# Optimization experiments

Hardware: AMD Instinct MI355X
Metric: run time of the kernel (lower is better)

The kernel has to match this reference:

```python
import jax, jax.numpy as jnp
import numpy as np

N = 50000      # nodes
E = 800000     # edges (before self-loops)
IN = 64        # in_channels
HID = 128      # hidden_channels
EPS = 1e-5     # BatchNorm eps


def _bn(x, g, b):
    # eval-mode BatchNorm with running_mean=0, running_var=1
    return x * (g / np.float32(np.sqrt(1.0 + EPS))) + b


def _gat(x, src, dst, W, a_s, a_d, bias, heads, outc):
    # PyG GATConv: lin -> per-node attention logits -> edge softmax over dst -> scatter-sum
    n = x.shape[0]
    xh = (x @ W).reshape(n, heads, outc)                    # [N,H,C]
    al_s = (xh * a_s[None]).sum(-1)                          # [N,H]
    al_d = (xh * a_d[None]).sum(-1)                          # [N,H]
    alpha = jax.nn.leaky_relu(al_s[src] + al_d[dst], 0.2)    # [E2,H]
    amax = jax.ops.segment_max(alpha, dst, num_segments=n)   # segment softmax (stable)
    ex = jnp.exp(alpha - amax[dst])
    den = jax.ops.segment_sum(ex, dst, num_segments=n)
    w = ex / den[dst]                                        # [E2,H]
    out = jax.ops.segment_sum(xh[src] * w[:, :, None], dst, num_segments=n)
    return out.reshape(n, heads * outc) + bias


def setup_inputs() -> dict:
    key = jax.random.key(0)
    ks = jax.random.split(key, 40)
    nrm = lambda k, s, sc=0.05: jax.random.normal(k, s, jnp.float32) * sc
    inp = {}
    inp['x'] = jax.random.normal(ks[0], (N, IN), jnp.float32)
    inp['edge_index'] = jax.random.randint(ks[1], (2, E), 0, N, dtype=jnp.int64)
    inp['Wp'] = nrm(ks[2], (IN, HID)); inp['bp'] = jnp.zeros((HID,), jnp.float32)
    # layer 0/1: heads=4, out=32; layer 2: heads=1, out=128
    C4 = HID // 4
    inp['W0'] = nrm(ks[3], (HID, HID)); inp['as0'] = nrm(ks[4], (4, C4)); inp['ad0'] = nrm(ks[5], (4, C4)); inp['b0'] = jnp.zeros((HID,), jnp.float32)
    inp['g0'] = jnp.ones((HID,), jnp.float32); inp['be0'] = jnp.zeros((HID,), jnp.float32)
    inp['W1'] = nrm(ks[6], (HID, HID)); inp['as1'] = nrm(ks[7], (4, C4)); inp['ad1'] = nrm(ks[8], (4, C4)); inp['b1'] = jnp.zeros((HID,), jnp.float32)
    inp['g1'] = jnp.ones((HID,), jnp.float32); inp['be1'] = jnp.zeros((HID,), jnp.float32)
    inp['W2'] = nrm(ks[9], (HID, HID)); inp['as2'] = nrm(ks[10], (1, HID)); inp['ad2'] = nrm(ks[11], (1, HID)); inp['b2'] = jnp.zeros((HID,), jnp.float32)
    inp['g2'] = jnp.ones((HID,), jnp.float32); inp['be2'] = jnp.zeros((HID,), jnp.float32)
    inp['fi'] = jnp.ones((HID,), jnp.float32)
    inp['Wc1'] = nrm(ks[12], (HID, HID // 2)); inp['bc1'] = jnp.zeros((HID // 2,), jnp.float32)
    inp['gc'] = jnp.ones((HID // 2,), jnp.float32); inp['bec'] = jnp.zeros((HID // 2,), jnp.float32)
    inp['Wc2'] = nrm(ks[13], (HID // 2, HID // 4)); inp['bc2'] = jnp.zeros((HID // 4,), jnp.float32)
    inp['Wc3'] = nrm(ks[14], (HID // 4, 2)); inp['bc3'] = jnp.zeros((2,), jnp.float32)
    return inp


def reference(x, edge_index, Wp, bp, W0, as0, ad0, b0, g0, be0, W1, as1, ad1, b1, g1, be1, W2, as2, ad2, b2, g2, be2, fi, Wc1, bc1, gc, bec, Wc2, bc2, Wc3, bc3):
    n = x.shape[0]
    loops = jnp.arange(n, dtype=edge_index.dtype)  # GATConv add_self_loops=True
    src = jnp.concatenate([edge_index[0], loops])
    dst = jnp.concatenate([edge_index[1], loops])
    h = x @ Wp + bp
    h = jax.nn.elu(_bn(_gat(h, src, dst, W0, as0, ad0, b0, 4, HID // 4), g0, be0))
    h = jax.nn.elu(_bn(_gat(h, src, dst, W1, as1, ad1, b1, 4, HID // 4), g1, be1))
    h = jax.nn.elu(_bn(_gat(h, src, dst, W2, as2, ad2, b2, 1, HID), g2, be2))
    h = h * fi
    h = jax.nn.relu(h @ Wc1 + bc1)
    h = _bn(h, gc, bec)
    h = jax.nn.relu(h @ Wc2 + bc2)
    return h @ Wc3 + bc3
```

## Files before the change

kernel.cpp:

```cpp
#include <hip/hip_runtime.h>
#include <math.h>

#define NFEAT 128
#define INF   64
#define BN_RSQ 0.99999500003749937f

template <int K, int NT, int EPI>
__launch_bounds__(256)
__global__ void linear4_kernel(const float* __restrict__ in, const float* __restrict__ W,
                               const float* __restrict__ bias, const float* __restrict__ g,
                               const float* __restrict__ be, float* __restrict__ out, int n) {
    __shared__ float xs[64 * 68];
    __shared__ float wsm[64 * 68];
    const int tx = threadIdx.x & 15;
    const int ty = threadIdx.x >> 4;
    const int row0 = blockIdx.x * 64;
    const int col0 = blockIdx.y * 64;
    float acc[4][4] = {};
    for (int kc = 0; kc < K; kc += 64) {
        __syncthreads();
        for (int i = threadIdx.x; i < 1024; i += 256) {
            const int rr = i >> 4;
            const int k4 = (i & 15) << 2;
            const int row = row0 + rr;
            float4 v = make_float4(0.f, 0.f, 0.f, 0.f);
            if (row < n) v = *(const float4*)&in[(long)row * K + kc + k4];
            *(float4*)&xs[rr * 68 + k4] = v;
        }
        for (int i = threadIdx.x; i < 1024; i += 256) {
            const int kk = i >> 4;
            const int j4 = (i & 15) << 2;
            *(float4*)&wsm[kk * 68 + j4] =
                *(const float4*)&W[(long)(kc + kk) * NT + col0 + j4];
        }
        __syncthreads();
#pragma unroll 16
        for (int k = 0; k < 64; ++k) {
            const float4 wv = *(const float4*)&wsm[k * 68 + (tx << 2)];
            const float x0 = xs[(ty * 4 + 0) * 68 + k];
            const float x1 = xs[(ty * 4 + 1) * 68 + k];
            const float x2 = xs[(ty * 4 + 2) * 68 + k];
            const float x3 = xs[(ty * 4 + 3) * 68 + k];
            acc[0][0] = fmaf(x0, wv.x, acc[0][0]); acc[0][1] = fmaf(x0, wv.y, acc[0][1]);
            acc[0][2] = fmaf(x0, wv.z, acc[0][2]); acc[0][3] = fmaf(x0, wv.w, acc[0][3]);
            acc[1][0] = fmaf(x1, wv.x, acc[1][0]); acc[1][1] = fmaf(x1, wv.y, acc[1][1]);
            acc[1][2] = fmaf(x1, wv.z, acc[1][2]); acc[1][3] = fmaf(x1, wv.w, acc[1][3]);
            acc[2][0] = fmaf(x2, wv.x, acc[2][0]); acc[2][1] = fmaf(x2, wv.y, acc[2][1]);
            acc[2][2] = fmaf(x2, wv.z, acc[2][2]); acc[2][3] = fmaf(x2, wv.w, acc[2][3]);
            acc[3][0] = fmaf(x3, wv.x, acc[3][0]); acc[3][1] = fmaf(x3, wv.y, acc[3][1]);
            acc[3][2] = fmaf(x3, wv.z, acc[3][2]); acc[3][3] = fmaf(x3, wv.w, acc[3][3]);
        }
    }
    const int col = col0 + (tx << 2);
    float4 bv = make_float4(0.f, 0.f, 0.f, 0.f);
    if (bias) bv = *(const float4*)&bias[col];
    float4 gv, ev;
    if (EPI == 2) { gv = *(const float4*)&g[col]; ev = *(const float4*)&be[col]; }
#pragma unroll
    for (int i = 0; i < 4; ++i) {
        const int row = row0 + ty * 4 + i;
        if (row >= n) break;
        float4 v = make_float4(acc[i][0] + bv.x, acc[i][1] + bv.y,
                               acc[i][2] + bv.z, acc[i][3] + bv.w);
        if (EPI == 2) {
            v.x = fmaxf(v.x, 0.f) * (gv.x * BN_RSQ) + ev.x;
            v.y = fmaxf(v.y, 0.f) * (gv.y * BN_RSQ) + ev.y;
            v.z = fmaxf(v.z, 0.f) * (gv.z * BN_RSQ) + ev.z;
            v.w = fmaxf(v.w, 0.f) * (gv.w * BN_RSQ) + ev.w;
        }
        *(float4*)&out[(long)row * NT + col] = v;
    }
}

template <int K, int MT, int MFULL, int EPI, int ITERS>
__launch_bounds__(256)
__global__ void linear_kernel(const float* __restrict__ in, const float* __restrict__ W,
                              const float* __restrict__ bias, float* __restrict__ out, int n) {
    constexpr int RPI = 256 / MT;
    __shared__ float Wl[K * MT];
    __shared__ float xl[RPI * (K + 1)];
    for (int i = threadIdx.x; i < K * MT; i += 256)
        Wl[i] = W[(i / MT) * MFULL + (i % MT)];
    const int j = threadIdx.x % MT;
    const int r = threadIdx.x / MT;
    const int row0 = blockIdx.x * (RPI * ITERS);
    for (int it = 0; it < ITERS; ++it) {
        const int base = row0 + it * RPI;
        __syncthreads();
        for (int i = threadIdx.x; i < RPI * K; i += 256) {
            int rr = i / K, kk = i - rr * K;
            int row = base + rr;
            xl[rr * (K + 1) + kk] = (row < n) ? in[(long)row * K + kk] : 0.f;
        }
        __syncthreads();
        float acc = 0.f;
#pragma unroll
        for (int k = 0; k < K; ++k) acc += xl[r * (K + 1) + k] * Wl[k * MT + j];
        const int row = base + r;
        if (row < n) {
            float v = acc;
            if (bias) v += bias[j];
            if (EPI >= 1) v = fmaxf(v, 0.f);
            out[(long)row * MFULL + j] = v;
        }
    }
}

template <int H, int C>
__global__ void gat_logits_kernel(const float* __restrict__ xh, const float* __restrict__ a_s,
                                  const float* __restrict__ a_d, float* __restrict__ als,
                                  float* __restrict__ ald, int n) {
    int idx = blockIdx.x * blockDim.x + threadIdx.x;
    if (idx >= n * H) return;
    int node = idx / H, h = idx - node * H;
    const float4* xp  = (const float4*)(xh + (long)node * NFEAT + h * C);
    const float4* asp = (const float4*)(a_s + h * C);
    const float4* adp = (const float4*)(a_d + h * C);
    float ss = 0.f, sd = 0.f;
#pragma unroll
    for (int c = 0; c < C / 4; ++c) {
        float4 v = xp[c], a = asp[c], b = adp[c];
        ss += v.x * a.x + v.y * a.y + v.z * a.z + v.w * a.w;
        sd += v.x * b.x + v.y * b.y + v.z * b.z + v.w * b.w;
    }
    als[idx] = ss;
    ald[idx] = sd;
}

__global__ void zero_int_kernel(int* __restrict__ p, int n) {
    int i = blockIdx.x * blockDim.x + threadIdx.x;
    if (i < n) p[i] = 0;
}

__global__ void hist_kernel(const int* __restrict__ ei, int E, int n, int* __restrict__ deg) {
    int e = blockIdx.x * blockDim.x + threadIdx.x;
    if (e >= E + n) return;
    int d = (e < E) ? ei[E + e] : (e - E);
    atomicAdd(&deg[d], 1);
}

__global__ void scanA_kernel(const int* __restrict__ deg, int n,
                             int* __restrict__ rowptr, int* __restrict__ bsum) {
    __shared__ int s[256];
    int t = threadIdx.x;
    int idx = blockIdx.x * 256 + t;
    s[t] = (idx < n) ? deg[idx] : 0;
    __syncthreads();
    for (int o = 1; o < 256; o <<= 1) {
        int x = (t >= o) ? s[t - o] : 0;
        __syncthreads();
        s[t] += x;
        __syncthreads();
    }
    if (idx < n) rowptr[idx + 1] = s[t];
    if (t == 255) bsum[blockIdx.x] = s[255];
}

__global__ void scanB_kernel(int* __restrict__ bsum, int nb) {
    __shared__ int s[256];
    int t = threadIdx.x;
    s[t] = (t < nb) ? bsum[t] : 0;
    __syncthreads();
    for (int o = 1; o < 256; o <<= 1) {
        int x = (t >= o) ? s[t - o] : 0;
        __syncthreads();
        s[t] += x;
        __syncthreads();
    }
    if (t < nb) bsum[t] = s[t];
}

__global__ void scanC_kernel(const int* __restrict__ deg, int n, int* __restrict__ rowptr,
                             const int* __restrict__ bsum, int* __restrict__ cursor) {
    int idx = blockIdx.x * 256 + threadIdx.x;
    if (idx >= n) return;
    int off = (blockIdx.x > 0) ? bsum[blockIdx.x - 1] : 0;
    int val = rowptr[idx + 1] + off;
    rowptr[idx + 1] = val;
    cursor[idx] = val - deg[idx];
    if (idx == 0) rowptr[0] = 0;
}

__global__ void scatter_kernel(const int* __restrict__ ei, int E, int n,
                               int* __restrict__ cursor, int* __restrict__ csr_src) {
    int e = blockIdx.x * blockDim.x + threadIdx.x;
    if (e >= E + n) return;
    int s, d;
    if (e < E) { s = ei[e]; d = ei[E + e]; } else { s = e - E; d = s; }
    int pos = atomicAdd(&cursor[d], 1);
    csr_src[pos] = s;
}

template <int H>
__launch_bounds__(256)
__global__ void gat_gather_kernel(const int* __restrict__ rowptr, const int* __restrict__ csr_src,
                                  const float* __restrict__ xh, const float* __restrict__ als,
                                  const float* __restrict__ ald, const float* __restrict__ bias,
                                  const float* __restrict__ g, const float* __restrict__ be,
                                  const float* __restrict__ post, float* __restrict__ hout, int n) {
    const int lane = threadIdx.x & 63;
    const int d = blockIdx.x * 4 + (threadIdx.x >> 6);
    if (d >= n) return;
    const int c0 = lane, c1 = lane + 64;
    const int h0 = (H == 4) ? (lane >> 5) : 0;
    const int h1 = (H == 4) ? (h0 + 2) : 0;
    const float ad0 = ald[d * H + h0];
    const float ad1 = ald[d * H + h1];
    const int rs = rowptr[d], re = rowptr[d + 1];
    float den0 = 0.f, den1 = 0.f, acc0 = 0.f, acc1 = 0.f;
    for (int base = rs; base < re; base += 64) {
        int sv = 0;
        if (base + lane < re) sv = csr_src[base + lane];
        const int cnt = min(64, re - base);
        int s = __shfl(sv, 0, 64);
        float a0 = als[s * H + h0];
        float a1 = als[s * H + h1];
        float x0 = xh[(long)s * NFEAT + c0];
        float x1 = xh[(long)s * NFEAT + c1];
        for (int t = 0; t < cnt; ++t) {
            const float ca0 = a0, ca1 = a1, cx0 = x0, cx1 = x1;
            if (t + 1 < cnt) {
                const int sn = __shfl(sv, t + 1, 64);
                a0 = als[sn * H + h0];
                a1 = als[sn * H + h1];
                x0 = xh[(long)sn * NFEAT + c0];
                x1 = xh[(long)sn * NFEAT + c1];
            }
            float l0 = ca0 + ad0, l1 = ca1 + ad1;
            l0 = l0 > 0.f ? l0 : 0.2f * l0;
            l1 = l1 > 0.f ? l1 : 0.2f * l1;
            const float w0 = __expf(l0), w1 = __expf(l1);
            den0 += w0;                den1 += w1;
            acc0 = fmaf(w0, cx0, acc0); acc1 = fmaf(w1, cx1, acc1);
        }
    }
    float v0 = (acc0 / den0 + bias[c0]) * (g[c0] * BN_RSQ) + be[c0];
    float v1 = (acc1 / den1 + bias[c1]) * (g[c1] * BN_RSQ) + be[c1];
    v0 = v0 > 0.f ? v0 : expm1f(v0);
    v1 = v1 > 0.f ? v1 : expm1f(v1);
    if (post) { v0 *= post[c0]; v1 *= post[c1]; }
    hout[(long)d * NFEAT + c0] = v0;
    hout[(long)d * NFEAT + c1] = v1;
}

template <int H>
static void run_gat_layer(const float* hin, float* xh, float* als, float* ald,
                          const int* rowptr, const int* csr_src, int n,
                          const float* W, const float* as_, const float* ad_, const float* b,
                          const float* g, const float* be, const float* post, float* hout,
                          hipStream_t stream) {
    constexpr int C = NFEAT / H;
    dim3 grid((n + 63) / 64, 2);
    linear4_kernel<128, 128, 0><<<grid, 256, 0, stream>>>(hin, W, nullptr, nullptr, nullptr, xh, n);
    gat_logits_kernel<H, C><<<(n * H + 255) / 256, 256, 0, stream>>>(xh, as_, ad_, als, ald, n);
    gat_gather_kernel<H><<<(n + 3) / 4, 256, 0, stream>>>(rowptr, csr_src, xh, als, ald,
                                                          b, g, be, post, hout, n);
}

extern "C" void kernel_launch(void* const* d_in, const int* in_sizes, int n_in,
                              void* d_out, int out_size, void* d_ws, size_t ws_size,
                              hipStream_t stream) {
    const float* x   = (const float*)d_in[0];
    const int*   ei  = (const int*)d_in[1];
    const float* Wp  = (const float*)d_in[2];
    const float* bp  = (const float*)d_in[3];
    const float* W0  = (const float*)d_in[4];
    const float* as0 = (const float*)d_in[5];
    const float* ad0 = (const float*)d_in[6];
    const float* b0  = (const float*)d_in[7];
    const float* g0  = (const float*)d_in[8];
    const float* be0 = (const float*)d_in[9];
    const float* W1  = (const float*)d_in[10];
    const float* as1 = (const float*)d_in[11];
    const float* ad1 = (const float*)d_in[12];
    const float* b1  = (const float*)d_in[13];
    const float* g1  = (const float*)d_in[14];
    const float* be1 = (const float*)d_in[15];
    const float* W2  = (const float*)d_in[16];
    const float* as2 = (const float*)d_in[17];
    const float* ad2 = (const float*)d_in[18];
    const float* b2  = (const float*)d_in[19];
    const float* g2  = (const float*)d_in[20];
    const float* be2 = (const float*)d_in[21];
    const float* fi  = (const float*)d_in[22];
    const float* Wc1 = (const float*)d_in[23];
    const float* bc1 = (const float*)d_in[24];
    const float* gc  = (const float*)d_in[25];
    const float* bec = (const float*)d_in[26];
    const float* Wc2 = (const float*)d_in[27];
    const float* bc2 = (const float*)d_in[28];
    const float* Wc3 = (const float*)d_in[29];
    const float* bc3 = (const float*)d_in[30];

    const int n  = in_sizes[0] / INF;
    const int E  = in_sizes[1] / 2;
    const int E2 = E + n;
    const int NB = (n + 255) / 256;

    float* ws   = (float*)d_ws;
    float* h    = ws;
    float* xh   = h + (long)n * NFEAT;
    float* als  = xh + (long)n * NFEAT;
    float* ald  = als + (long)n * 4;
    int* deg     = (int*)(ald + (long)n * 4);
    int* rowptr  = deg + n;
    int* cursor  = rowptr + (n + 1);
    int* csr_src = cursor + n;
    int* bsum    = csr_src + (long)E2;

    zero_int_kernel<<<NB, 256, 0, stream>>>(deg, n);
    hist_kernel<<<(E2 + 255) / 256, 256, 0, stream>>>(ei, E, n, deg);
    scanA_kernel<<<NB, 256, 0, stream>>>(deg, n, rowptr, bsum);
    scanB_kernel<<<1, 256, 0, stream>>>(bsum, NB);
    scanC_kernel<<<NB, 256, 0, stream>>>(deg, n, rowptr, bsum, cursor);
    scatter_kernel<<<(E2 + 255) / 256, 256, 0, stream>>>(ei, E, n, cursor, csr_src);

    {
        dim3 grid((n + 63) / 64, 2);
        linear4_kernel<64, 128, 0><<<grid, 256, 0, stream>>>(x, Wp, bp, nullptr, nullptr, h, n);
    }

    run_gat_layer<4>(h, xh, als, ald, rowptr, csr_src, n, W0, as0, ad0, b0, g0, be0, nullptr, h, stream);
    run_gat_layer<4>(h, xh, als, ald, rowptr, csr_src, n, W1, as1, ad1, b1, g1, be1, nullptr, h, stream);
    run_gat_layer<1>(h, xh, als, ald, rowptr, csr_src, n, W2, as2, ad2, b2, g2, be2, fi, h, stream);

    {
        dim3 grid((n + 63) / 64, 1);
        linear4_kernel<128, 64, 2><<<grid, 256, 0, stream>>>(h, Wc1, bc1, gc, bec, xh, n);
    }
    linear_kernel<64, 32, 32, 1, 8><<<(n + 63) / 64, 256, 0, stream>>>(xh, Wc2, bc2, h, n);
    linear_kernel<32, 2, 2, 0, 2><<<(n + 255) / 256, 256, 0, stream>>>(h, Wc3, bc3, (float*)d_out, n);
}
```

Measured before the change: 645.2 us.

## Precompute edge weights per lane in LDS and add 128x128 register-tiled GEMM

After: 633.1 us. Within noise of the previous version (-1.9%).

```diff
diff --git a/kernel.cpp b/kernel.cpp
--- a/kernel.cpp
+++ b/kernel.cpp
@@ -4,6 +4,73 @@
 #define NFEAT 128
 #define INF   64
 #define BN_RSQ 0.99999500003749937f
+
+template <int K>
+__launch_bounds__(256)
+__global__ void linear8_kernel(const float* __restrict__ in, const float* __restrict__ W,
+                               const float* __restrict__ bias, float* __restrict__ out, int n) {
+    __shared__ float xs[128 * 36];
+    __shared__ float wt[128 * 36];
+    const int tid = threadIdx.x;
+    const int tx = tid & 15;
+    const int ty = tid >> 4;
+    const int row0 = blockIdx.x * 128;
+    float acc[8][8] = {};
+    for (int kc = 0; kc < K; kc += 32) {
+        __syncthreads();
+#pragma unroll
+        for (int r = 0; r < 4; ++r) {
+            const int idx = tid + 256 * r;
+            const int rr = idx >> 3;
+            const int k4 = (idx & 7) << 2;
+            const int row = row0 + rr;
+            float4 v = make_float4(0.f, 0.f, 0.f, 0.f);
+            if (row < n) v = *(const float4*)&in[(long)row * K + kc + k4];
+            *(float4*)&xs[rr * 36 + k4] = v;
+        }
+#pragma unroll
+        for (int r = 0; r < 4; ++r) {
+            const int idx = tid + 256 * r;
+            const int kk = idx >> 5;
+            const int c4 = (idx & 31) << 2;
+            const float4 v = *(const float4*)&W[(long)(kc + kk) * 128 + c4];
+            wt[(c4 + 0) * 36 + kk] = v.x;
+            wt[(c4 + 1) * 36 + kk] = v.y;
+            wt[(c4 + 2) * 36 + kk] = v.z;
+            wt[(c4 + 3) * 36 + kk] = v.w;
+        }
+        __syncthreads();
+#pragma unroll 2
+        for (int k4 = 0; k4 < 32; k4 += 4) {
+            float4 xa[8], wa[8];
+#pragma unroll
+            for (int i = 0; i < 8; ++i) xa[i] = *(const float4*)&xs[(ty + 16 * i) * 36 + k4];
+#pragma unroll
+            for (int j = 0; j < 8; ++j) wa[j] = *(const float4*)&wt[(tx + 16 * j) * 36 + k4];
+#pragma unroll
+            for (int i = 0; i < 8; ++i)
+#pragma unroll
+                for (int j = 0; j < 8; ++j) {
+                    acc[i][j] = fmaf(xa[i].x, wa[j].x, acc[i][j]);
+                    acc[i][j] = fmaf(xa[i].y, wa[j].y, acc[i][j]);
+                    acc[i][j] = fmaf(xa[i].z, wa[j].z, acc[i][j]);
+                    acc[i][j] = fmaf(xa[i].w, wa[j].w, acc[i][j]);
+                }
+        }
+    }
+#pragma unroll
+    for (int i = 0; i < 8; ++i) {
+        const int row = row0 + ty + 16 * i;
+        if (row >= n) continue;
+#pragma unroll
+        for (int j = 0; j < 8; ++j) {
+            const int col = tx + 16 * j;
+            float v = acc[i][j];
+            if (bias) v += bias[col];
+            out[(long)row * 128 + col] = v;
+        }
+    }
+}
 
 template <int K, int NT, int EPI>
 __launch_bounds__(256)
@@ -198,40 +265,65 @@
                                   const float* __restrict__ ald, const float* __restrict__ bias,
                                   const float* __restrict__ g, const float* __restrict__ be,
                                   const float* __restrict__ post, float* __restrict__ hout, int n) {
+    __shared__ int   slds[4][64];
+    __shared__ float wlds[4][64][H];
     const int lane = threadIdx.x & 63;
-    const int d = blockIdx.x * 4 + (threadIdx.x >> 6);
+    const int wid  = threadIdx.x >> 6;
+    const int d = blockIdx.x * 4 + wid;
     if (d >= n) return;
     const int c0 = lane, c1 = lane + 64;
     const int h0 = (H == 4) ? (lane >> 5) : 0;
     const int h1 = (H == 4) ? (h0 + 2) : 0;
-    const float ad0 = ald[d * H + h0];
-    const float ad1 = ald[d * H + h1];
+    float4 adv;
+    if (H == 4) adv = *(const float4*)&ald[d * 4];
+    else        adv.x = ald[d];
     const int rs = rowptr[d], re = rowptr[d + 1];
     float den0 = 0.f, den1 = 0.f, acc0 = 0.f, acc1 = 0.f;
     for (int base = rs; base < re; base += 64) {
+        const bool valid = (base + lane) < re;
         int sv = 0;
-        if (base + lane < re) sv = csr_src[base + lane];
-        const int cnt = min(64, re - base);
-        int s = __shfl(sv, 0, 64);
-        float a0 = als[s * H + h0];
-        float a1 = als[s * H + h1];
-        float x0 = xh[(long)s * NFEAT + c0];
-        float x1 = xh[(long)s * NFEAT + c1];
-        for (int t = 0; t < cnt; ++t) {
-            const float ca0 = a0, ca1 = a1, cx0 = x0, cx1 = x1;
-            if (t + 1 < cnt) {
-                const int sn = __shfl(sv, t + 1, 64);
-                a0 = als[sn * H + h0];
-                a1 = als[sn * H + h1];
-                x0 = xh[(long)sn * NFEAT + c0];
-                x1 = xh[(long)sn * NFEAT + c1];
-            }
-            float l0 = ca0 + ad0, l1 = ca1 + ad1;
+        if (valid) sv = csr_src[base + lane];
+        if (H == 4) {
+            const float4 a = *(const float4*)&als[sv * 4];
+            float l0 = a.x + adv.x, l1 = a.y + adv.y, l2 = a.z + adv.z, l3 = a.w + adv.w;
             l0 = l0 > 0.f ? l0 : 0.2f * l0;
             l1 = l1 > 0.f ? l1 : 0.2f * l1;
-            const float w0 = __expf(l0), w1 = __expf(l1);
-            den0 += w0;                den1 += w1;
-            acc0 = fmaf(w0, cx0, acc0); acc1 = fmaf(w1, cx1, acc1);
+            l2 = l2 > 0.f ? l2 : 0.2f * l2;
+            l3 = l3 > 0.f ? l3 : 0.2f * l3;
+            float4 wv;
+            wv.x = valid ? __expf(l0) : 0.f;
+            wv.y = valid ? __expf(l1) : 0.f;
+            wv.z = valid ? __expf(l2) : 0.f;
+            wv.w = valid ? __expf(l3) : 0.f;
+            slds[wid][lane] = sv;
+            *(float4*)&wlds[wid][lane][0] = wv;
+        } else {
+            float l = als[sv] + adv.x;
+            l = l > 0.f ? l : 0.2f * l;
+            slds[wid][lane] = sv;
+            wlds[wid][lane][0] = valid ? __expf(l) : 0.f;
+        }
+        const int cnt = min(64, re - base);
+        const int cnt2 = (cnt + 1) & ~1;
+        for (int t = 0; t < cnt2; t += 2) {
+            const int sa = slds[wid][t];
+            const int sb = slds[wid][t + 1];
+            float wa0, wa1, wb0, wb1;
+            if (H == 4) {
+                wa0 = wlds[wid][t][h0];     wa1 = wlds[wid][t][h1];
+                wb0 = wlds[wid][t + 1][h0]; wb1 = wlds[wid][t + 1][h1];
+            } else {
+                wa0 = wlds[wid][t][0];      wa1 = wa0;
+                wb0 = wlds[wid][t + 1][0];  wb1 = wb0;
+            }
+            const float xa0 = xh[(long)sa * NFEAT + c0];
+            const float xa1 = xh[(long)sa * NFEAT + c1];
+            const float xb0 = xh[(long)sb * NFEAT + c0];
+            const float xb1 = xh[(long)sb * NFEAT + c1];
+            den0 += wa0 + wb0;
+            den1 += wa1 + wb1;
+            acc0 = fmaf(wa0, xa0, acc0); acc0 = fmaf(wb0, xb0, acc0);
+            acc1 = fmaf(wa1, xa1, acc1); acc1 = fmaf(wb1, xb1, acc1);
         }
     }
     float v0 = (acc0 / den0 + bias[c0]) * (g[c0] * BN_RSQ) + be[c0];
@@ -250,8 +342,7 @@
                           const float* g, const float* be, const float* post, float* hout,
                           hipStream_t stream) {
     constexpr int C = NFEAT / H;
-    dim3 grid((n + 63) / 64, 2);
-    linear4_kernel<128, 128, 0><<<grid, 256, 0, stream>>>(hin, W, nullptr, nullptr, nullptr, xh, n);
+    linear8_kernel<128><<<(n + 127) / 128, 256, 0, stream>>>(hin, W, nullptr, xh, n);
     gat_logits_kernel<H, C><<<(n * H + 255) / 256, 256, 0, stream>>>(xh, as_, ad_, als, ald, n);
     gat_gather_kernel<H><<<(n + 3) / 4, 256, 0, stream>>>(rowptr, csr_src, xh, als, ald,
                                                           b, g, be, post, hout, n);
@@ -315,10 +406,7 @@
     scanC_kernel<<<NB, 256, 0, stream>>>(deg, n, rowptr, bsum, cursor);
     scatter_kernel<<<(E2 + 255) / 256, 256, 0, stream>>>(ei, E, n, cursor, csr_src);
 
-    {
-        dim3 grid((n + 63) / 64, 2);
-        linear4_kernel<64, 128, 0><<<grid, 256, 0, stream>>>(x, Wp, bp, nullptr, nullptr, h, n);
-    }
+    linear8_kernel<64><<<(n + 127) / 128, 256, 0, stream>>>(x, Wp, bp, h, n);
 
     run_gat_layer<4>(h, xh, als, ald, rowptr, csr_src, n, W0, as0, ad0, b0, g0, be0, nullptr, h, stream);
     run_gat_layer<4>(h, xh, als, ald, rowptr, csr_src, n, W1, as1, ad1, b1, g1, be1, nullptr, h, stream);
```
